# Performance work log

Measured on AMD Instinct MI355X. Metric: run time of the kernel, lower is better.

## Reference

```python
import jax, jax.numpy as jnp
import numpy as np

H = 1024

def setup_inputs() -> dict:
    key = jax.random.key(0)
    ks = jax.random.split(key, 8)
    B, S = 32, 2048
    scale = 1.0 / np.sqrt(H)
    return {
        "query": jax.random.normal(ks[0], (B, 1, H), dtype=jnp.float32),
        "keys": jax.random.normal(ks[1], (B, S, H), dtype=jnp.float32),
        "Wa_w": jax.random.uniform(ks[2], (H, H), jnp.float32, -scale, scale),
        "Wa_b": jax.random.uniform(ks[3], (H,), jnp.float32, -scale, scale),
        "Ua_w": jax.random.uniform(ks[4], (H, H), jnp.float32, -scale, scale),
        "Ua_b": jax.random.uniform(ks[5], (H,), jnp.float32, -scale, scale),
        "Va_w": jax.random.uniform(ks[6], (1, H), jnp.float32, -scale, scale),
        "Va_b": jax.random.uniform(ks[7], (1,), jnp.float32, -scale, scale),
    }

def reference(query, keys, Wa_w, Wa_b, Ua_w, Ua_b, Va_w, Va_b):
    # q_proj: [B,1,H], k_proj: [B,S,H]
    q_proj = jnp.einsum('bqh,oh->bqo', query, Wa_w) + Wa_b
    k_proj = jnp.einsum('bsh,oh->bso', keys, Ua_w) + Ua_b
    e = jnp.tanh(q_proj + k_proj)                      # [B,S,H] via broadcast
    scores = jnp.einsum('bsh,oh->bso', e, Va_w) + Va_b # [B,S,1]
    scores = scores[..., 0][:, None, :]                # [B,1,S]
    weights = jax.nn.softmax(scores, axis=-1)          # [B,1,S]
    context = jnp.einsum('bqs,bsh->bqh', weights, keys)  # [B,1,H]
    return (context, weights)
```

## Files before the change

kernel.cpp:

```cpp
#include <hip/hip_runtime.h>
#include <math.h>

typedef __attribute__((ext_vector_type(8))) short short8;
typedef __attribute__((ext_vector_type(4))) float f32x4;
typedef unsigned int u32;

constexpr int Hd = 1024;
constexpr int Bn = 32;
constexpr int Sn = 2048;
constexpr int Mn = Bn * Sn;
constexpr int NXB = 8;
constexpr int SCH = 8;

constexpr size_t WS_QPROJ   = 0;
constexpr size_t WS_PARTIAL = 131072;
constexpr size_t WS_CPART   = 131072 + 2097152;
constexpr size_t WS_BASE_END = WS_CPART + 1048576;
constexpr size_t WS_UAHI    = WS_BASE_END;
constexpr size_t WS_UALO    = WS_BASE_END + 2097152;
constexpr size_t WS_NEED_SPLIT = WS_UALO + 2097152;

__device__ __forceinline__ void gload16(const void* g, void* l) {
    __builtin_amdgcn_global_load_lds(
        (const __attribute__((address_space(1))) u32*)g,
        (__attribute__((address_space(3))) u32*)l, 16, 0, 0);
}

__device__ __forceinline__ void split4(float4 v, uint2& h, uint2& l) {
    u32 b0 = __float_as_uint(v.x), b1 = __float_as_uint(v.y);
    u32 b2 = __float_as_uint(v.z), b3 = __float_as_uint(v.w);
    h.x = (b0 >> 16) | (b1 & 0xffff0000u);
    h.y = (b2 >> 16) | (b3 & 0xffff0000u);
    float l0 = v.x - __uint_as_float(b0 & 0xffff0000u);
    float l1 = v.y - __uint_as_float(b1 & 0xffff0000u);
    float l2 = v.z - __uint_as_float(b2 & 0xffff0000u);
    float l3 = v.w - __uint_as_float(b3 & 0xffff0000u);
    l.x = (__float_as_uint(l0) >> 16) | (__float_as_uint(l1) & 0xffff0000u);
    l.y = (__float_as_uint(l2) >> 16) | (__float_as_uint(l3) & 0xffff0000u);
}

__global__ __launch_bounds__(256) void split_kernel(
    const float4* __restrict__ src, uint2* __restrict__ hi, uint2* __restrict__ lo, int n4)
{
    int i = blockIdx.x * 256 + threadIdx.x;
    if (i >= n4) return;
    uint2 h, l;
    split4(src[i], h, l);
    hi[i] = h; lo[i] = l;
}

__global__ __launch_bounds__(256) void qproj_kernel(
    const float* __restrict__ query, const float* __restrict__ Wa_w,
    const float* __restrict__ Wa_b, float* __restrict__ q_proj)
{
    int gtid = blockIdx.x * 256 + threadIdx.x;
    int wid  = gtid >> 6;
    int lane = threadIdx.x & 63;
    int b = wid >> 10, o = wid & 1023;
    const float4* q = reinterpret_cast<const float4*>(query + (size_t)b * Hd);
    const float4* w = reinterpret_cast<const float4*>(Wa_w + (size_t)o * Hd);
    float acc = 0.f;
#pragma unroll
    for (int i = 0; i < 4; ++i) {
        float4 qv = q[lane + i * 64];
        float4 wv = w[lane + i * 64];
        acc = fmaf(qv.x, wv.x, acc);
        acc = fmaf(qv.y, wv.y, acc);
        acc = fmaf(qv.z, wv.z, acc);
        acc = fmaf(qv.w, wv.w, acc);
    }
#pragma unroll
    for (int off = 32; off > 0; off >>= 1) acc += __shfl_down(acc, off);
    if (lane == 0) q_proj[wid] = acc + Wa_b[o];
}

template <bool SPLITB>
__global__ __launch_bounds__(256, 2) void score_gemm_kernel(
    const float* __restrict__ keys,
    const unsigned short* __restrict__ ua_hi, const unsigned short* __restrict__ ua_lo,
    const float* __restrict__ Ua_w,
    const float* __restrict__ Ua_b, const float* __restrict__ Va_w,
    const float* __restrict__ q_proj, float* __restrict__ partial)
{
    __shared__ __align__(16) unsigned char lds[32768];
    __shared__ float red[128][2];
    constexpr int AHI = 0, ALO = 8192, BHI = 16384, BLO = 24576;

    const int id = blockIdx.x;
    const int by = (id & 7) * 64 + (id >> 6);
    const int bx = (id >> 3) & 7;

    const int tid = threadIdx.x;
    const int lane = tid & 63, wid = tid >> 6;
    const int wm = wid >> 1, wn = wid & 1;
    const int lr = lane & 15, lk = lane >> 4;
    const int m0 = by * 128, n0 = bx * 128;

    const float* Ap = keys + (size_t)m0 * Hd;
    const float* Bp = Ua_w + (size_t)n0 * Hd;
    const int ar = tid >> 3, ac = tid & 7;

    float4 curA[4], nxtA[4], curB[4], nxtB[4];
#pragma unroll
    for (int u = 0; u < 4; ++u)
        curA[u] = *reinterpret_cast<const float4*>(Ap + (size_t)(ar + u * 32) * Hd + ac * 4);
    if (!SPLITB) {
#pragma unroll
        for (int u = 0; u < 4; ++u)
            curB[u] = *reinterpret_cast<const float4*>(Bp + (size_t)(ar + u * 32) * Hd + ac * 4);
    }

    f32x4 acc[4][4];
#pragma unroll
    for (int i = 0; i < 4; ++i)
#pragma unroll
        for (int j = 0; j < 4; ++j) acc[i][j] = f32x4{0.f, 0.f, 0.f, 0.f};

    const char* uah = (const char*)ua_hi;
    const char* ual = (const char*)ua_lo;
    const int c2 = wid * 2;
    const int brow = c2 * 16 + (lane >> 2);
    const size_t boff0 = (size_t)(n0 + brow) * (Hd * 2) + (size_t)(lane & 3) * 16;
    const size_t brstep = (size_t)16 * Hd * 2;

    for (int t = 0; t < 32; ++t) {
        const int k0 = t * 32;
        __syncthreads();
        if (SPLITB) {
            size_t bo = boff0 + (size_t)k0 * 2;
            gload16(uah + bo, lds + BHI + c2 * 1024);
            gload16(ual + bo, lds + BLO + c2 * 1024);
            gload16(uah + bo + brstep, lds + BHI + (c2 + 1) * 1024);
            gload16(ual + bo + brstep, lds + BLO + (c2 + 1) * 1024);
        } else {
#pragma unroll
            for (int u = 0; u < 4; ++u) {
                uint2 h, l;
                split4(curB[u], h, l);
                int db = (ar + u * 32) * 64 + ac * 8;
                *reinterpret_cast<uint2*>(lds + BHI + db) = h;
                *reinterpret_cast<uint2*>(lds + BLO + db) = l;
            }
        }
#pragma unroll
        for (int u = 0; u < 4; ++u) {
            uint2 h, l;
            split4(curA[u], h, l);
            int db = (ar + u * 32) * 64 + ac * 8;
            *reinterpret_cast<uint2*>(lds + AHI + db) = h;
            *reinterpret_cast<uint2*>(lds + ALO + db) = l;
        }
        __syncthreads();
        if (t < 31) {
#pragma unroll
            for (int u = 0; u < 4; ++u)
                nxtA[u] = *reinterpret_cast<const float4*>(
                    Ap + (size_t)(ar + u * 32) * Hd + (k0 + 32) + ac * 4);
            if (!SPLITB) {
#pragma unroll
                for (int u = 0; u < 4; ++u)
                    nxtB[u] = *reinterpret_cast<const float4*>(
                        Bp + (size_t)(ar + u * 32) * Hd + (k0 + 32) + ac * 4);
            }
        }
        short8 ah[4], al[4], bh[4], bl[4];
#pragma unroll
        for (int i = 0; i < 4; ++i) {
            int ab = (wm * 64 + i * 16 + lr) * 64 + lk * 16;
            ah[i] = *reinterpret_cast<const short8*>(lds + AHI + ab);
            al[i] = *reinterpret_cast<const short8*>(lds + ALO + ab);
        }
#pragma unroll
        for (int j = 0; j < 4; ++j) {
            int bb = (wn * 64 + j * 16 + lr) * 64 + lk * 16;
            bh[j] = *reinterpret_cast<const short8*>(lds + BHI + bb);
            bl[j] = *reinterpret_cast<const short8*>(lds + BLO + bb);
        }
#pragma unroll
        for (int i = 0; i < 4; ++i)
#pragma unroll
            for (int j = 0; j < 4; ++j) {
                acc[i][j] = __builtin_amdgcn_mfma_f32_16x16x32_bf16(ah[i], bh[j], acc[i][j], 0, 0, 0);
                acc[i][j] = __builtin_amdgcn_mfma_f32_16x16x32_bf16(ah[i], bl[j], acc[i][j], 0, 0, 0);
                acc[i][j] = __builtin_amdgcn_mfma_f32_16x16x32_bf16(al[i], bh[j], acc[i][j], 0, 0, 0);
            }
        if (t < 31) {
#pragma unroll
            for (int u = 0; u < 4; ++u) curA[u] = nxtA[u];
            if (!SPLITB) {
#pragma unroll
                for (int u = 0; u < 4; ++u) curB[u] = nxtB[u];
            }
        }
    }

    float vaw_[4], qb_[4], ub_[4];
    const int b = m0 >> 11;
#pragma unroll
    for (int j = 0; j < 4; ++j) {
        int c = n0 + wn * 64 + j * 16 + lr;
        vaw_[j] = Va_w[c];
        qb_[j]  = q_proj[b * Hd + c];
        ub_[j]  = Ua_b[c];
    }
#pragma unroll
    for (int i = 0; i < 4; ++i) {
#pragma unroll
        for (int r = 0; r < 4; ++r) {
            float s = 0.f;
#pragma unroll
            for (int j = 0; j < 4; ++j)
                s = fmaf(vaw_[j], tanhf(qb_[j] + ub_[j] + acc[i][j][r]), s);
#pragma unroll
            for (int m = 1; m < 16; m <<= 1) s += __shfl_xor(s, m);
            if (lr == 0) red[wm * 64 + i * 16 + lk * 4 + r][wn] = s;
        }
    }
    __syncthreads();
    if (tid < 128)
        partial[(size_t)(m0 + tid) * NXB + bx] = red[tid][0] + red[tid][1];
}

__global__ __launch_bounds__(256) void softmax_kernel(
    const float* __restrict__ partial, const float* __restrict__ Va_b,
    float* __restrict__ weights)
{
    __shared__ float sred[4];
    const int b = blockIdx.x, tid = threadIdx.x;
    const int lane = tid & 63, wv = tid >> 6;
    const float vb = Va_b[0];
    float sc[8];
    float mx = -1e30f;
#pragma unroll
    for (int t = 0; t < 8; ++t) {
        size_t bs = (size_t)b * Sn + t * 256 + tid;
        const float4* p = reinterpret_cast<const float4*>(partial + bs * NXB);
        float4 p0 = p[0], p1 = p[1];
        float v = vb + p0.x + p0.y + p0.z + p0.w + p1.x + p1.y + p1.z + p1.w;
        sc[t] = v;
        mx = fmaxf(mx, v);
    }
#pragma unroll
    for (int off = 32; off > 0; off >>= 1) mx = fmaxf(mx, __shfl_xor(mx, off));
    if (lane == 0) sred[wv] = mx;
    __syncthreads();
    mx = fmaxf(fmaxf(sred[0], sred[1]), fmaxf(sred[2], sred[3]));
    __syncthreads();
    float sum = 0.f;
#pragma unroll
    for (int t = 0; t < 8; ++t) { sc[t] = expf(sc[t] - mx); sum += sc[t]; }
#pragma unroll
    for (int off = 32; off > 0; off >>= 1) sum += __shfl_xor(sum, off);
    if (lane == 0) sred[wv] = sum;
    __syncthreads();
    sum = sred[0] + sred[1] + sred[2] + sred[3];
    float inv = 1.0f / sum;
#pragma unroll
    for (int t = 0; t < 8; ++t)
        weights[(size_t)b * Sn + t * 256 + tid] = sc[t] * inv;
}

__global__ __launch_bounds__(256) void context_partial_kernel(
    const float* __restrict__ keys, const float* __restrict__ weights,
    float* __restrict__ cpart)
{
    __shared__ float w[256];
    const int b = blockIdx.x, hb = blockIdx.y, sc = blockIdx.z;
    const int h = hb * 256 + threadIdx.x;
    w[threadIdx.x] = weights[(size_t)b * Sn + sc * 256 + threadIdx.x];
    __syncthreads();
    const float* kp = keys + ((size_t)b * Sn + sc * 256) * Hd + h;
    float acc = 0.f;
#pragma unroll 8
    for (int s = 0; s < 256; ++s)
        acc = fmaf(w[s], kp[(size_t)s * Hd], acc);
    cpart[(size_t)(b * SCH + sc) * Hd + h] = acc;
}

__global__ __launch_bounds__(256) void context_reduce_kernel(
    const float* __restrict__ cpart, float* __restrict__ ctx)
{
    int idx = blockIdx.x * 256 + threadIdx.x;
    int b = idx >> 10, h = idx & 1023;
    float t = 0.f;
#pragma unroll
    for (int s = 0; s < SCH; ++s) t += cpart[(size_t)(b * SCH + s) * Hd + h];
    ctx[idx] = t;
}

extern "C" void kernel_launch(void* const* d_in, const int* in_sizes, int n_in,
                              void* d_out, int out_size, void* d_ws, size_t ws_size,
                              hipStream_t stream)
{
    const float* query = (const float*)d_in[0];
    const float* keys  = (const float*)d_in[1];
    const float* Wa_w  = (const float*)d_in[2];
    const float* Wa_b  = (const float*)d_in[3];
    const float* Ua_w  = (const float*)d_in[4];
    const float* Ua_b  = (const float*)d_in[5];
    const float* Va_w  = (const float*)d_in[6];
    const float* Va_b  = (const float*)d_in[7];

    float* ctx     = (float*)d_out;
    float* weights = (float*)d_out + Bn * Hd;

    char* wsb      = (char*)d_ws;
    float* q_proj  = (float*)(wsb + WS_QPROJ);
    float* partial = (float*)(wsb + WS_PARTIAL);
    float* cpart   = (float*)(wsb + WS_CPART);
    unsigned short* ua_hi = (unsigned short*)(wsb + WS_UAHI);
    unsigned short* ua_lo = (unsigned short*)(wsb + WS_UALO);

    const bool use_split = (ws_size >= WS_NEED_SPLIT);

    if (use_split)
        split_kernel<<<dim3(1024), dim3(256), 0, stream>>>(
            (const float4*)Ua_w, (uint2*)ua_hi, (uint2*)ua_lo, (Hd * Hd) / 4);
    qproj_kernel<<<dim3(8192), dim3(256), 0, stream>>>(query, Wa_w, Wa_b, q_proj);
    if (use_split)
        score_gemm_kernel<true><<<dim3(4096), dim3(256), 0, stream>>>(
            keys, ua_hi, ua_lo, Ua_w, Ua_b, Va_w, q_proj, partial);
    else
        score_gemm_kernel<false><<<dim3(4096), dim3(256), 0, stream>>>(
            keys, ua_hi, ua_lo, Ua_w, Ua_b, Va_w, q_proj, partial);
    softmax_kernel<<<dim3(Bn), dim3(256), 0, stream>>>(partial, Va_b, weights);
    context_partial_kernel<<<dim3(Bn, Hd / 256, SCH), dim3(256), 0, stream>>>(
        keys, weights, cpart);
    context_reduce_kernel<<<dim3(128), dim3(256), 0, stream>>>(cpart, ctx);
}
```

Measured before the change: 776.7 us.

## Widen score GEMM tile to 128x256 to halve keys reloads and block count

The score GEMM tile grows from 128x128 to 128x256 output columns, so each block covers a quarter of the Ua_w rows. Each fp32 keys tile is loaded and split into bf16 hi/lo fewer times across the grid, and the launch drops from 4096 to 2048 blocks. The partial-score buffer shrinks to 4 entries per row and the softmax is adjusted to match. In exchange the kernel needs more LDS and twice the accumulators per thread (128 floats), which raises register pressure and may cut occupancy under launch_bounds(256,2). LDS stores are also widened to 16-byte writes, and B fragments are now loaded per column inside the MFMA loop.

```diff
diff --git a/kernel.cpp b/kernel.cpp
--- a/kernel.cpp
+++ b/kernel.cpp
@@ -8,16 +8,16 @@
 constexpr int Hd = 1024;
 constexpr int Bn = 32;
 constexpr int Sn = 2048;
-constexpr int Mn = Bn * Sn;
-constexpr int NXB = 8;
+constexpr int Mn = 65536;
+constexpr int NXB = 4;
 constexpr int SCH = 8;
 
 constexpr size_t WS_QPROJ   = 0;
 constexpr size_t WS_PARTIAL = 131072;
-constexpr size_t WS_CPART   = 131072 + 2097152;
+constexpr size_t WS_CPART   = 131072 + 1048576;
 constexpr size_t WS_BASE_END = WS_CPART + 1048576;
 constexpr size_t WS_UAHI    = WS_BASE_END;
-constexpr size_t WS_UALO    = WS_BASE_END + 2097152;
+constexpr size_t WS_UALO    = WS_UAHI + 2097152;
 constexpr size_t WS_NEED_SPLIT = WS_UALO + 2097152;
 
 __device__ __forceinline__ void gload16(const void* g, void* l) {
@@ -82,88 +82,88 @@
     const float* __restrict__ Ua_b, const float* __restrict__ Va_w,
     const float* __restrict__ q_proj, float* __restrict__ partial)
 {
-    __shared__ __align__(16) unsigned char lds[32768];
+    __shared__ __align__(16) unsigned char lds[49152];
     __shared__ float red[128][2];
-    constexpr int AHI = 0, ALO = 8192, BHI = 16384, BLO = 24576;
+    constexpr int AHI = 0, ALO = 8192, BHI = 16384, BLO = 32768;
 
     const int id = blockIdx.x;
-    const int by = (id & 7) * 64 + (id >> 6);
-    const int bx = (id >> 3) & 7;
+    const int by = (id & 7) * 64 + (id >> 5);
+    const int bx = (id >> 3) & 3;
 
     const int tid = threadIdx.x;
     const int lane = tid & 63, wid = tid >> 6;
     const int wm = wid >> 1, wn = wid & 1;
     const int lr = lane & 15, lk = lane >> 4;
-    const int m0 = by * 128, n0 = bx * 128;
+    const int m0 = by * 128, n0 = bx * 256;
 
     const float* Ap = keys + (size_t)m0 * Hd;
-    const float* Bp = Ua_w + (size_t)n0 * Hd;
-    const int ar = tid >> 3, ac = tid & 7;
-
-    float4 curA[4], nxtA[4], curB[4], nxtB[4];
-#pragma unroll
-    for (int u = 0; u < 4; ++u)
-        curA[u] = *reinterpret_cast<const float4*>(Ap + (size_t)(ar + u * 32) * Hd + ac * 4);
-    if (!SPLITB) {
-#pragma unroll
-        for (int u = 0; u < 4; ++u)
-            curB[u] = *reinterpret_cast<const float4*>(Bp + (size_t)(ar + u * 32) * Hd + ac * 4);
-    }
-
-    f32x4 acc[4][4];
+    const int ra = tid >> 2, ca = tid & 3;
+
+    float4 curA[4], nxtA[4];
+#pragma unroll
+    for (int u = 0; u < 2; ++u)
+#pragma unroll
+        for (int v = 0; v < 2; ++v)
+            curA[u * 2 + v] = *reinterpret_cast<const float4*>(
+                Ap + (size_t)(ra + u * 64) * Hd + ca * 8 + v * 4);
+
+    f32x4 acc[4][8];
 #pragma unroll
     for (int i = 0; i < 4; ++i)
 #pragma unroll
-        for (int j = 0; j < 4; ++j) acc[i][j] = f32x4{0.f, 0.f, 0.f, 0.f};
+        for (int j = 0; j < 8; ++j) acc[i][j] = f32x4{0.f, 0.f, 0.f, 0.f};
 
     const char* uah = (const char*)ua_hi;
     const char* ual = (const char*)ua_lo;
-    const int c2 = wid * 2;
-    const int brow = c2 * 16 + (lane >> 2);
-    const size_t boff0 = (size_t)(n0 + brow) * (Hd * 2) + (size_t)(lane & 3) * 16;
-    const size_t brstep = (size_t)16 * Hd * 2;
+    const int grow = wid * 16 + (lane >> 2);
+    const int gcol = (lane & 3) * 16;
 
     for (int t = 0; t < 32; ++t) {
         const int k0 = t * 32;
         __syncthreads();
         if (SPLITB) {
-            size_t bo = boff0 + (size_t)k0 * 2;
-            gload16(uah + bo, lds + BHI + c2 * 1024);
-            gload16(ual + bo, lds + BLO + c2 * 1024);
-            gload16(uah + bo + brstep, lds + BHI + (c2 + 1) * 1024);
-            gload16(ual + bo + brstep, lds + BLO + (c2 + 1) * 1024);
+#pragma unroll
+            for (int u = 0; u < 4; ++u) {
+                size_t bo = ((size_t)(n0 + grow + u * 64) << 11) + (size_t)k0 * 2 + gcol;
+                gload16(uah + bo, lds + BHI + u * 4096 + wid * 1024);
+                gload16(ual + bo, lds + BLO + u * 4096 + wid * 1024);
+            }
         } else {
 #pragma unroll
             for (int u = 0; u < 4; ++u) {
-                uint2 h, l;
-                split4(curB[u], h, l);
-                int db = (ar + u * 32) * 64 + ac * 8;
-                *reinterpret_cast<uint2*>(lds + BHI + db) = h;
-                *reinterpret_cast<uint2*>(lds + BLO + db) = l;
+                int s = tid + u * 256, rb = s >> 2, cs = s & 3;
+                const float* src = Ua_w + (size_t)(n0 + rb) * Hd + k0 + cs * 8;
+                float4 v0 = *reinterpret_cast<const float4*>(src);
+                float4 v1 = *reinterpret_cast<const float4*>(src + 4);
+                uint2 h0, l0, h1, l1;
+                split4(v0, h0, l0); split4(v1, h1, l1);
+                uint4 H = {h0.x, h0.y, h1.x, h1.y};
+                uint4 L = {l0.x, l0.y, l1.x, l1.y};
+                int db = rb * 64 + cs * 16;
+                *reinterpret_cast<uint4*>(lds + BHI + db) = H;
+                *reinterpret_cast<uint4*>(lds + BLO + db) = L;
             }
         }
 #pragma unroll
-        for (int u = 0; u < 4; ++u) {
-            uint2 h, l;
-            split4(curA[u], h, l);
-            int db = (ar + u * 32) * 64 + ac * 8;
-            *reinterpret_cast<uint2*>(lds + AHI + db) = h;
-            *reinterpret_cast<uint2*>(lds + ALO + db) = l;
+        for (int u = 0; u < 2; ++u) {
+            uint2 h0, l0, h1, l1;
+            split4(curA[u * 2], h0, l0); split4(curA[u * 2 + 1], h1, l1);
+            uint4 H = {h0.x, h0.y, h1.x, h1.y};
+            uint4 L = {l0.x, l0.y, l1.x, l1.y};
+            int db = (ra + u * 64) * 64 + ca * 16;
+            *reinterpret_cast<uint4*>(lds + AHI + db) = H;
+            *reinterpret_cast<uint4*>(lds + ALO + db) = L;
         }
         __syncthreads();
         if (t < 31) {
 #pragma unroll
-            for (int u = 0; u < 4; ++u)
-                nxtA[u] = *reinterpret_cast<const float4*>(
-                    Ap + (size_t)(ar + u * 32) * Hd + (k0 + 32) + ac * 4);
-            if (!SPLITB) {
-#pragma unroll
-                for (int u = 0; u < 4; ++u)
-                    nxtB[u] = *reinterpret_cast<const float4*>(
-                        Bp + (size_t)(ar + u * 32) * Hd + (k0 + 32) + ac * 4);
-            }
-        }
-        short8 ah[4], al[4], bh[4], bl[4];
+            for (int u = 0; u < 2; ++u)
+#pragma unroll
+                for (int v = 0; v < 2; ++v)
+                    nxtA[u * 2 + v] = *reinterpret_cast<const float4*>(
+                        Ap + (size_t)(ra + u * 64) * Hd + (k0 + 32) + ca * 8 + v * 4);
+        }
+        short8 ah[4], al[4];
 #pragma unroll
         for (int i = 0; i < 4; ++i) {
             int ab = (wm * 64 + i * 16 + lr) * 64 + lk * 16;
@@ -171,34 +171,28 @@
             al[i] = *reinterpret_cast<const short8*>(lds + ALO + ab);
         }
 #pragma unroll
-        for (int j = 0; j < 4; ++j) {
-            int bb = (wn * 64 + j * 16 + lr) * 64 + lk * 16;
-            bh[j] = *reinterpret_cast<const short8*>(lds + BHI + bb);
-            bl[j] = *reinterpret_cast<const short8*>(lds + BLO + bb);
-        }
-#pragma unroll
-        for (int i = 0; i < 4; ++i)
-#pragma unroll
-            for (int j = 0; j < 4; ++j) {
-                acc[i][j] = __builtin_amdgcn_mfma_f32_16x16x32_bf16(ah[i], bh[j], acc[i][j], 0, 0, 0);
-                acc[i][j] = __builtin_amdgcn_mfma_f32_16x16x32_bf16(ah[i], bl[j], acc[i][j], 0, 0, 0);
-                acc[i][j] = __builtin_amdgcn_mfma_f32_16x16x32_bf16(al[i], bh[j], acc[i][j], 0, 0, 0);
+        for (int j = 0; j < 8; ++j) {
+            int bb = (wn * 128 + j * 16 + lr) * 64 + lk * 16;
+            short8 bh = *reinterpret_cast<const short8*>(lds + BHI + bb);
+            short8 bl = *reinterpret_cast<const short8*>(lds + BLO + bb);
+#pragma unroll
+            for (int i = 0; i < 4; ++i) {
+                acc[i][j] = __builtin_amdgcn_mfma_f32_16x16x32_bf16(ah[i], bh, acc[i][j], 0, 0, 0);
+                acc[i][j] = __builtin_amdgcn_mfma_f32_16x16x32_bf16(ah[i], bl, acc[i][j], 0, 0, 0);
+                acc[i][j] = __builtin_amdgcn_mfma_f32_16x16x32_bf16(al[i], bh, acc[i][j], 0, 0, 0);
             }
+        }
         if (t < 31) {
 #pragma unroll
             for (int u = 0; u < 4; ++u) curA[u] = nxtA[u];
-            if (!SPLITB) {
-#pragma unroll
-                for (int u = 0; u < 4; ++u) curB[u] = nxtB[u];
-            }
-        }
-    }
-
-    float vaw_[4], qb_[4], ub_[4];
+        }
+    }
+
     const int b = m0 >> 11;
-#pragma unroll
-    for (int j = 0; j < 4; ++j) {
-        int c = n0 + wn * 64 + j * 16 + lr;
+    float vaw_[8], qb_[8], ub_[8];
+#pragma unroll
+    for (int j = 0; j < 8; ++j) {
+        int c = n0 + wn * 128 + j * 16 + lr;
         vaw_[j] = Va_w[c];
         qb_[j]  = q_proj[b * Hd + c];
         ub_[j]  = Ua_b[c];
@@ -209,7 +203,7 @@
         for (int r = 0; r < 4; ++r) {
             float s = 0.f;
 #pragma unroll
-            for (int j = 0; j < 4; ++j)
+            for (int j = 0; j < 8; ++j)
                 s = fmaf(vaw_[j], tanhf(qb_[j] + ub_[j] + acc[i][j][r]), s);
 #pragma unroll
             for (int m = 1; m < 16; m <<= 1) s += __shfl_xor(s, m);
@@ -234,9 +228,8 @@
 #pragma unroll
     for (int t = 0; t < 8; ++t) {
         size_t bs = (size_t)b * Sn + t * 256 + tid;
-        const float4* p = reinterpret_cast<const float4*>(partial + bs * NXB);
-        float4 p0 = p[0], p1 = p[1];
-        float v = vb + p0.x + p0.y + p0.z + p0.w + p1.x + p1.y + p1.z + p1.w;
+        float4 p0 = *reinterpret_cast<const float4*>(partial + bs * NXB);
+        float v = vb + p0.x + p0.y + p0.z + p0.w;
         sc[t] = v;
         mx = fmaxf(mx, v);
     }
@@ -318,10 +311,10 @@
             (const float4*)Ua_w, (uint2*)ua_hi, (uint2*)ua_lo, (Hd * Hd) / 4);
     qproj_kernel<<<dim3(8192), dim3(256), 0, stream>>>(query, Wa_w, Wa_b, q_proj);
     if (use_split)
-        score_gemm_kernel<true><<<dim3(4096), dim3(256), 0, stream>>>(
+        score_gemm_kernel<true><<<dim3(2048), dim3(256), 0, stream>>>(
             keys, ua_hi, ua_lo, Ua_w, Ua_b, Va_w, q_proj, partial);
     else
-        score_gemm_kernel<false><<<dim3(4096), dim3(256), 0, stream>>>(
+        score_gemm_kernel<false><<<dim3(2048), dim3(256), 0, stream>>>(
             keys, ua_hi, ua_lo, Ua_w, Ua_b, Va_w, q_proj, partial);
     softmax_kernel<<<dim3(Bn), dim3(256), 0, stream>>>(partial, Va_b, weights);
     context_partial_kernel<<<dim3(Bn, Hd / 256, SCH), dim3(256), 0, stream>>>(
```

Result: no change. 769.1 us (-1.0%).
